# Kernel optimization log

Measured on AMD Instinct MI355X. Metric: run time of the kernel, lower is better.

## Reference

```python
import jax, jax.numpy as jnp
import numpy as np

# P parts, each with IN=4 input columns; hidden=16, out=3 per the module.
P, IN, H, O = 16, 4, 16, 3
NEG_SLOPE = 0.01  # nn.LeakyReLU default
BN_EPS = 1e-5


def setup_inputs() -> dict:
    key = jax.random.key(0)
    ks = jax.random.split(key, 6)
    b, n, f = 256, 64, 512
    x = jax.random.normal(ks[0], (b, n, f), dtype=jnp.float32)
    # part_list: 16 contiguous groups of 4 node indices
    parts = jnp.arange(n, dtype=jnp.int32).reshape(P, IN)
    # Xavier-normal linear weights, bias filled with 0.1 (per init_weights)
    W1 = jax.random.normal(ks[1], (P, IN, H), dtype=jnp.float32) * np.float32((2.0 / (IN + H)) ** 0.5)
    b1 = jnp.full((P, H), 0.1, dtype=jnp.float32)
    W2 = jax.random.normal(ks[2], (P, H, O), dtype=jnp.float32) * np.float32((2.0 / (H + O)) ** 0.5)
    b2 = jnp.full((P, O), 0.1, dtype=jnp.float32)
    # BatchNorm1d(3): weight=1, bias=0; eval mode uses running stats (randomized here so BN is non-trivial)
    gamma = jnp.ones((P, O), dtype=jnp.float32)
    beta = jnp.zeros((P, O), dtype=jnp.float32)
    mean = jax.random.normal(ks[3], (P, O), dtype=jnp.float32) * 0.1
    var = jax.random.uniform(ks[4], (P, O), dtype=jnp.float32, minval=0.5, maxval=1.5)
    return {"x": x, "parts": parts, "W1": W1, "b1": b1, "W2": W2, "b2": b2,
            "gamma": gamma, "beta": beta, "mean": mean, "var": var}


def reference(x, parts, W1, b1, W2, b2, gamma, beta, mean, var):
    # Eval-mode forward (Dropout = identity, BatchNorm uses running stats).
    b, n, f = x.shape
    xr = jnp.transpose(x, (0, 2, 1)).reshape(-1, n)      # [R, n], R = b*f
    xp = xr[:, parts]                                     # gather -> [R, P, IN]
    h = jnp.einsum('rpi,pih->rph', xp, W1) + b1           # grouped GEMM 1
    h = jax.nn.leaky_relu(h, NEG_SLOPE)
    y = jnp.einsum('rph,pho->rpo', h, W2) + b2            # grouped GEMM 2 -> [R, P, O]
    y = (y - mean) * jax.lax.rsqrt(var + BN_EPS) * gamma + beta
    y = jax.nn.leaky_relu(y, NEG_SLOPE)
    # torch.cat along dim=-1 of per-part [R,3] blocks == part-major reshape
    y = y.reshape(b, f, -1)                               # [b, f, P*O]
    return jnp.transpose(y, (0, 2, 1))                    # [b, P*O, f]
```

## Files before the change

### kernel.cpp

```cpp
#include <hip/hip_runtime.h>

#define NPARTS 16
#define NIN 4
#define NH 16
#define NO 3
#define NEG_SLOPE 0.01f
#define BN_EPS 1e-5f
#define NN 64
#define NF 512
#define NF4 (NF / 4)

__device__ __forceinline__ float leaky1(float a) {
    return fmaf(fminf(a, 0.0f), NEG_SLOPE - 1.0f, a);
}
__device__ __forceinline__ float4 leaky4(float4 a) {
    a.x = leaky1(a.x); a.y = leaky1(a.y); a.z = leaky1(a.z); a.w = leaky1(a.w);
    return a;
}
__device__ __forceinline__ float4 fma4s(float4 v, float s, float4 d) {
    d.x = fmaf(v.x, s, d.x); d.y = fmaf(v.y, s, d.y);
    d.z = fmaf(v.z, s, d.z); d.w = fmaf(v.w, s, d.w);
    return d;
}
__device__ __forceinline__ float4 splat4(float s) {
    float4 r; r.x = s; r.y = s; r.z = s; r.w = s; return r;
}

__global__ __launch_bounds__(128)
void agg_joint_kernel(const float* __restrict__ x,
                      const int* __restrict__ parts,
                      const float* __restrict__ W1,
                      const float* __restrict__ b1,
                      const float* __restrict__ W2,
                      const float* __restrict__ b2,
                      const float* __restrict__ gamma,
                      const float* __restrict__ beta,
                      const float* __restrict__ mean,
                      const float* __restrict__ var,
                      float* __restrict__ out)
{
    const int p  = blockIdx.x & (NPARTS - 1);
    const int bi = blockIdx.x >> 4;
    const int t  = threadIdx.x;

    __shared__ float s_w1[NIN * NH];
    __shared__ float s_b1[NH];
    __shared__ float s_w2[NH * NO];
    __shared__ float s_shift[NO];
    __shared__ int   s_nidx[NIN];

    if (t < NIN * NH) s_w1[t] = W1[p * NIN * NH + t];
    if (t < NH)       s_b1[t] = b1[p * NH + t];
    if (t < NH * NO) {
        const int o = t % NO;
        const float sc = gamma[p * NO + o] * rsqrtf(var[p * NO + o] + BN_EPS);
        s_w2[t] = W2[p * NH * NO + t] * sc;
    }
    if (t < NO) {
        const float sc = gamma[p * NO + t] * rsqrtf(var[p * NO + t] + BN_EPS);
        s_shift[t] = (b2[p * NO + t] - mean[p * NO + t]) * sc + beta[p * NO + t];
    }
    if (t < NIN) s_nidx[t] = parts[p * NIN + t];
    __syncthreads();

    float4 xv[NIN];
#pragma unroll
    for (int j = 0; j < NIN; ++j) {
        const float4* xr =
            (const float4*)(x + ((size_t)bi * NN + s_nidx[j]) * NF);
        xv[j] = xr[t];
    }

    float4 acc[NO];
#pragma unroll
    for (int o = 0; o < NO; ++o) acc[o] = splat4(s_shift[o]);

#pragma unroll
    for (int k = 0; k < NH; ++k) {
        float4 h = splat4(s_b1[k]);
#pragma unroll
        for (int j = 0; j < NIN; ++j) h = fma4s(xv[j], s_w1[j * NH + k], h);
        h = leaky4(h);
#pragma unroll
        for (int o = 0; o < NO; ++o) acc[o] = fma4s(h, s_w2[k * NO + o], acc[o]);
    }

    float4* ob = (float4*)(out + ((size_t)bi * (NPARTS * NO) + p * NO) * NF);
#pragma unroll
    for (int o = 0; o < NO; ++o) ob[(size_t)o * NF4 + t] = leaky4(acc[o]);
}

extern "C" void kernel_launch(void* const* d_in, const int* in_sizes, int n_in,
                              void* d_out, int out_size, void* d_ws, size_t ws_size,
                              hipStream_t stream) {
    const float* x     = (const float*)d_in[0];
    const int*   parts = (const int*)d_in[1];
    const float* W1    = (const float*)d_in[2];
    const float* b1    = (const float*)d_in[3];
    const float* W2    = (const float*)d_in[4];
    const float* b2    = (const float*)d_in[5];
    const float* gamma = (const float*)d_in[6];
    const float* beta  = (const float*)d_in[7];
    const float* mean  = (const float*)d_in[8];
    const float* var   = (const float*)d_in[9];
    float* out = (float*)d_out;

    const int batch = in_sizes[0] / (NN * NF);
    dim3 grid(batch * NPARTS);
    dim3 block(128);
    agg_joint_kernel<<<grid, block, 0, stream>>>(
        x, parts, W1, b1, W2, b2, gamma, beta, mean, var, out);
}
```

Measured before the change: 100.4 us.

## Process two batch items per block with nontemporal loads/stores and packed weights

```diff
diff --git a/kernel.cpp b/kernel.cpp
--- a/kernel.cpp
+++ b/kernel.cpp
@@ -9,6 +9,20 @@
 #define NN 64
 #define NF 512
 #define NF4 (NF / 4)
+#define IPB 2
+
+typedef float f32x4 __attribute__((ext_vector_type(4)));
+union F4u { float4 f; f32x4 v; };
+
+__device__ __forceinline__ float4 ntload4(const float4* p) {
+    F4u u;
+    u.v = __builtin_nontemporal_load(reinterpret_cast<const f32x4*>(p));
+    return u.f;
+}
+__device__ __forceinline__ void ntstore4(float4* p, float4 x) {
+    F4u u; u.f = x;
+    __builtin_nontemporal_store(u.v, reinterpret_cast<f32x4*>(p));
+}
 
 __device__ __forceinline__ float leaky1(float a) {
     return fmaf(fminf(a, 0.0f), NEG_SLOPE - 1.0f, a);
@@ -39,55 +53,78 @@
                       const float* __restrict__ var,
                       float* __restrict__ out)
 {
-    const int p  = blockIdx.x & (NPARTS - 1);
-    const int bi = blockIdx.x >> 4;
-    const int t  = threadIdx.x;
+    const int p   = blockIdx.x & (NPARTS - 1);
+    const int bi0 = (blockIdx.x >> 4) * IPB;
+    const int t   = threadIdx.x;
 
-    __shared__ float s_w1[NIN * NH];
-    __shared__ float s_b1[NH];
-    __shared__ float s_w2[NH * NO];
+    const int4 nidx = *reinterpret_cast<const int4*>(parts + p * NIN);
+
+    float4 xv[IPB][NIN];
+    const float4* xf = reinterpret_cast<const float4*>(x);
+#pragma unroll
+    for (int i = 0; i < IPB; ++i) {
+        const size_t rb = (size_t)(bi0 + i) * NN;
+        xv[i][0] = ntload4(xf + (rb + (size_t)nidx.x) * NF4 + t);
+        xv[i][1] = ntload4(xf + (rb + (size_t)nidx.y) * NF4 + t);
+        xv[i][2] = ntload4(xf + (rb + (size_t)nidx.z) * NF4 + t);
+        xv[i][3] = ntload4(xf + (rb + (size_t)nidx.w) * NF4 + t);
+    }
+
+    __shared__ __align__(16) float s_pack[NH][8];
     __shared__ float s_shift[NO];
-    __shared__ int   s_nidx[NIN];
-
-    if (t < NIN * NH) s_w1[t] = W1[p * NIN * NH + t];
-    if (t < NH)       s_b1[t] = b1[p * NH + t];
-    if (t < NH * NO) {
-        const int o = t % NO;
-        const float sc = gamma[p * NO + o] * rsqrtf(var[p * NO + o] + BN_EPS);
-        s_w2[t] = W2[p * NH * NO + t] * sc;
+    {
+        const int k   = t >> 3;
+        const int idx = t & 7;
+        float wv;
+        if (idx < NIN) {
+            wv = W1[(p * NIN + idx) * NH + k];
+        } else if (idx < 7) {
+            const int o = idx - NIN;
+            wv = W2[(p * NH + k) * NO + o] *
+                 (gamma[p * NO + o] * rsqrtf(var[p * NO + o] + BN_EPS));
+        } else {
+            wv = b1[p * NH + k];
+        }
+        s_pack[k][idx] = wv;
+        if (t < NO) {
+            const float sc = gamma[p * NO + t] * rsqrtf(var[p * NO + t] + BN_EPS);
+            s_shift[t] = (b2[p * NO + t] - mean[p * NO + t]) * sc + beta[p * NO + t];
+        }
     }
-    if (t < NO) {
-        const float sc = gamma[p * NO + t] * rsqrtf(var[p * NO + t] + BN_EPS);
-        s_shift[t] = (b2[p * NO + t] - mean[p * NO + t]) * sc + beta[p * NO + t];
-    }
-    if (t < NIN) s_nidx[t] = parts[p * NIN + t];
     __syncthreads();
 
-    float4 xv[NIN];
+    float4 acc[IPB][NO];
 #pragma unroll
-    for (int j = 0; j < NIN; ++j) {
-        const float4* xr =
-            (const float4*)(x + ((size_t)bi * NN + s_nidx[j]) * NF);
-        xv[j] = xr[t];
-    }
-
-    float4 acc[NO];
+    for (int i = 0; i < IPB; ++i)
 #pragma unroll
-    for (int o = 0; o < NO; ++o) acc[o] = splat4(s_shift[o]);
+        for (int o = 0; o < NO; ++o) acc[i][o] = splat4(s_shift[o]);
 
 #pragma unroll
     for (int k = 0; k < NH; ++k) {
-        float4 h = splat4(s_b1[k]);
+        const float4 wa = *reinterpret_cast<const float4*>(&s_pack[k][0]);
+        const float4 wb = *reinterpret_cast<const float4*>(&s_pack[k][4]);
 #pragma unroll
-        for (int j = 0; j < NIN; ++j) h = fma4s(xv[j], s_w1[j * NH + k], h);
-        h = leaky4(h);
-#pragma unroll
-        for (int o = 0; o < NO; ++o) acc[o] = fma4s(h, s_w2[k * NO + o], acc[o]);
+        for (int i = 0; i < IPB; ++i) {
+            float4 h = splat4(wb.w);
+            h = fma4s(xv[i][0], wa.x, h);
+            h = fma4s(xv[i][1], wa.y, h);
+            h = fma4s(xv[i][2], wa.z, h);
+            h = fma4s(xv[i][3], wa.w, h);
+            h = leaky4(h);
+            acc[i][0] = fma4s(h, wb.x, acc[i][0]);
+            acc[i][1] = fma4s(h, wb.y, acc[i][1]);
+            acc[i][2] = fma4s(h, wb.z, acc[i][2]);
+        }
     }
 
-    float4* ob = (float4*)(out + ((size_t)bi * (NPARTS * NO) + p * NO) * NF);
+    float4* of = reinterpret_cast<float4*>(out);
 #pragma unroll
-    for (int o = 0; o < NO; ++o) ob[(size_t)o * NF4 + t] = leaky4(acc[o]);
+    for (int i = 0; i < IPB; ++i) {
+        float4* ob = of + ((size_t)(bi0 + i) * (NPARTS * NO) + p * NO) * NF4 + t;
+#pragma unroll
+        for (int o = 0; o < NO; ++o)
+            ntstore4(ob + (size_t)o * NF4, leaky4(acc[i][o]));
+    }
 }
 
 extern "C" void kernel_launch(void* const* d_in, const int* in_sizes, int n_in,
@@ -106,7 +143,7 @@
     float* out = (float*)d_out;
 
     const int batch = in_sizes[0] / (NN * NF);
-    dim3 grid(batch * NPARTS);
+    dim3 grid((batch / IPB) * NPARTS);
     dim3 block(128);
     agg_joint_kernel<<<grid, block, 0, stream>>>(
         x, parts, W1, b1, W2, b2, gamma, beta, mean, var, out);
```

Result: slower. 105.0 us (+4.6%).
